# Kernel optimization log

Measured on AMD Instinct MI355X. Metric: run time of the kernel, lower is better.

The kernel has to match this reference:

```python
import jax, jax.numpy as jnp
import numpy as np

B, SX, SC, D, H = 4, 2048, 2048, 512, 8
DK = D // H


def setup_inputs() -> dict:
    key = jax.random.key(0)
    ks = jax.random.split(key, 12)
    s = 0.02
    return {
        "x": jax.random.normal(ks[0], (B, SX, D), jnp.float32),
        "c": jax.random.normal(ks[1], (B, SC, D), jnp.float32),
        "Wq": jax.random.normal(ks[2], (D, D), jnp.float32) * s,
        "bq": jnp.zeros((D,), jnp.float32),
        "Wk": jax.random.normal(ks[3], (D, D), jnp.float32) * s,
        "bk": jnp.zeros((D,), jnp.float32),
        "Wv": jax.random.normal(ks[4], (D, D), jnp.float32) * s,
        "bv": jnp.zeros((D,), jnp.float32),
        "Wo": jax.random.normal(ks[5], (D, D), jnp.float32) * s,
        "bo": jnp.zeros((D,), jnp.float32),
        "rel_table": jax.random.normal(ks[6], (SX + SC - 1, H), jnp.float32) * s,
    }


def reference(x, c, Wq, bq, Wk, bk, Wv, bv, Wo, bo, rel_table):
    b = x.shape[0]
    # projections (torch Linear: y = x @ W.T + b)
    q = (x @ Wq.T + bq).reshape(b, SX, H, DK).transpose(0, 2, 1, 3)  # (B,H,Sx,dk)
    k = (c @ Wk.T + bk).reshape(b, SC, H, DK).transpose(0, 2, 1, 3)  # (B,H,Sc,dk)
    v = (c @ Wv.T + bv).reshape(b, SC, H, DK).transpose(0, 2, 1, 3)
    scale = 1.0 / jnp.sqrt(jnp.float32(DK))
    scores = jnp.einsum('bhqd,bhkd->bhqk', q, k) * scale  # (B,H,Sx,Sc)
    # relative position bias: index (Sx,Sc) into table (Sx+Sc-1, H)
    rel_idx = jnp.arange(SX)[:, None] - jnp.arange(SC)[None, :] + (SC - 1)
    bias = rel_table[rel_idx].transpose(2, 0, 1)  # (H,Sx,Sc)
    scores = scores + bias[None]
    # causal_mask=False -> False * -1e9 adds 0 (no-op); omitted
    weights = jax.nn.softmax(scores, axis=-1)
    out = jnp.einsum('bhqk,bhkd->bhqd', weights, v)  # (B,H,Sx,dk)
    out = out.transpose(0, 2, 1, 3).reshape(b, SX, D)
    return out @ Wo.T + bo
```

## Files before the change

### kernel.cpp

```cpp
#include <hip/hip_runtime.h>
#include <hip/hip_bf16.h>
#include <cstdint>
#include <cstddef>

typedef __bf16 bf16;
typedef __bf16 bf16x4 __attribute__((ext_vector_type(4)));
typedef __bf16 bf16x8 __attribute__((ext_vector_type(8)));
typedef float f32x4 __attribute__((ext_vector_type(4)));
typedef float f32x16 __attribute__((ext_vector_type(16)));

#define MFMA16(a, b, c) __builtin_amdgcn_mfma_f32_16x16x32_bf16((a), (b), (c), 0, 0, 0)
#define MFMA32(a, b, c) __builtin_amdgcn_mfma_f32_32x32x16_bf16((a), (b), (c), 0, 0, 0)
#define GLD16(g, l) __builtin_amdgcn_global_load_lds( \
    (const __attribute__((address_space(1))) void*)(g), \
    (__attribute__((address_space(3))) void*)(l), 16, 0, 0)

constexpr int Bsz = 4, SX = 2048, SC = 2048, Dm = 512, H = 8, DK = 64;
constexpr float L2E = 1.4426950408889634f;

__global__ __launch_bounds__(256) void cvt_weights(
    const float* __restrict__ Wq, const float* __restrict__ Wk,
    const float* __restrict__ Wv, const float* __restrict__ Wo,
    bf16* __restrict__ out)
{
    int i = (blockIdx.x * 256 + threadIdx.x) * 8;
    int w = i >> 18;
    int off = i & 262143;
    const float* src = (w == 0) ? Wq : (w == 1) ? Wk : (w == 2) ? Wv : Wo;
    float4 v0 = *(const float4*)(src + off);
    float4 v1 = *(const float4*)(src + off + 4);
    bf16x8 o = { (bf16)v0.x, (bf16)v0.y, (bf16)v0.z, (bf16)v0.w,
                 (bf16)v1.x, (bf16)v1.y, (bf16)v1.z, (bf16)v1.w };
    *(bf16x8*)(out + i) = o;
}

__global__ __launch_bounds__(256) void cvt_xc(
    const float* __restrict__ x, const float* __restrict__ c,
    bf16* __restrict__ out)
{
    int i = (blockIdx.x * 256 + threadIdx.x) * 8;
    const float* src = (i < 4194304) ? x : c;
    int off = i & 4194303;
    float4 v0 = *(const float4*)(src + off);
    float4 v1 = *(const float4*)(src + off + 4);
    bf16x8 o = { (bf16)v0.x, (bf16)v0.y, (bf16)v0.z, (bf16)v0.w,
                 (bf16)v1.x, (bf16)v1.y, (bf16)v1.z, (bf16)v1.w };
    *(bf16x8*)(out + i) = o;
}

__global__ __launch_bounds__(256) void cvt_rel(
    const float* __restrict__ rel, float* __restrict__ relT)
{
    int h = blockIdx.y;
    int i = blockIdx.x * 256 + threadIdx.x;
    if (i < SX + SC - 1) relT[h * (SX + SC - 1) + i] = rel[i * H + h] * L2E;
}

template <int MODE>
__global__ __launch_bounds__(256, 2) void proj_gemm(
    const bf16* __restrict__ A, const bf16* __restrict__ W,
    const float* __restrict__ bias, void* __restrict__ Yv)
{
    __shared__ alignas(16) bf16 As[128 * 64];
    __shared__ alignas(16) bf16 Bs[128 * 64];

    const int t = threadIdx.x;
    const int n0 = blockIdx.x * 128;
    const int m0 = blockIdx.y * 128;
    const int wid = t >> 6, lane = t & 63, lr = lane & 15, lq = lane >> 4;
    const int wm = (wid & 1) * 64, wn = (wid >> 1) * 64;

    const int rl = lane >> 3;
    const int ch = (lane & 7) ^ rl;

    f32x4 acc[4][4];
#pragma unroll
    for (int i = 0; i < 4; i++)
#pragma unroll
        for (int j = 0; j < 4; j++) acc[i][j] = f32x4{0.f, 0.f, 0.f, 0.f};

    for (int k0 = 0; k0 < Dm; k0 += 64) {
        const bf16* ga = A + (size_t)(m0 + wid * 32 + rl) * Dm + k0 + ch * 8;
        const bf16* gb = W + (size_t)(n0 + wid * 32 + rl) * Dm + k0 + ch * 8;
#pragma unroll
        for (int g = 0; g < 4; g++)
            GLD16(ga + (size_t)g * 8 * Dm, &As[(wid * 32 + g * 8) * 64]);
#pragma unroll
        for (int g = 0; g < 4; g++)
            GLD16(gb + (size_t)g * 8 * Dm, &Bs[(wid * 32 + g * 8) * 64]);
        __syncthreads();
#pragma unroll
        for (int ks = 0; ks < 2; ks++) {
            bf16x8 af[4], bfr[4];
#pragma unroll
            for (int mt = 0; mt < 4; mt++)
                af[mt] = *(const bf16x8*)&As[(wm + mt * 16 + lr) * 64 + (((ks * 4 + lq) ^ (lr & 7)) * 8)];
#pragma unroll
            for (int nt = 0; nt < 4; nt++)
                bfr[nt] = *(const bf16x8*)&Bs[(wn + nt * 16 + lr) * 64 + (((ks * 4 + lq) ^ (lr & 7)) * 8)];
#pragma unroll
            for (int mt = 0; mt < 4; mt++)
#pragma unroll
                for (int nt = 0; nt < 4; nt++)
                    acc[mt][nt] = MFMA16(af[mt], bfr[nt], acc[mt][nt]);
        }
        __syncthreads();
    }

#pragma unroll
    for (int mt = 0; mt < 4; mt++) {
#pragma unroll
        for (int nt = 0; nt < 4; nt++) {
#pragma unroll
            for (int r = 0; r < 4; r++) {
                int m = m0 + wm + mt * 16 + lq * 4 + r;
                int n = n0 + wn + nt * 16 + lr;
                float v = acc[mt][nt][r] + bias[n];
                int bh = (m >> 11) * 8 + (n >> 6);
                int key = m & 2047, dk = n & 63;
                if constexpr (MODE == 0) {
                    ((bf16*)Yv)[(size_t)(bh * 2048 + key) * 64 + dk] = (bf16)v;
                } else if constexpr (MODE == 3) {
                    int idx = ((((bh * 64 + (key >> 5)) * 4 + (dk >> 4)) * 2 + ((dk >> 3) & 1)) * 32
                               + (key & 31)) * 8 + (dk & 7);
                    ((bf16*)Yv)[idx] = (bf16)v;
                } else if constexpr (MODE == 4) {
                    int idx = (((((bh * 32 + (key >> 6)) * 4 + ((key >> 4) & 3)) * 2 + (dk >> 5)) * 2
                                + ((key >> 3) & 1)) * 32 + (dk & 31)) * 8 + (key & 7);
                    ((bf16*)Yv)[idx] = (bf16)v;
                } else {
                    ((float*)Yv)[(size_t)m * Dm + n] = v;
                }
            }
        }
    }
}

constexpr int PST = 72;

__global__ __launch_bounds__(128, 4) void attn_kernel(
    const bf16* __restrict__ Qm, const bf16* __restrict__ Kf,
    const bf16* __restrict__ Vf, const float* __restrict__ relT,
    bf16* __restrict__ Oa)
{
    const int id = blockIdx.x;
    const int xcd = id & 7, j = id >> 3;
    const int bh = xcd + 8 * (j & 3);
    const int q0 = (j >> 2) * 32;
    const int h = bh & 7, b = bh >> 3;
    const int t = threadIdx.x;
    const int wid = t >> 6, lane = t & 63;
    const int l31 = lane & 31, l5 = lane >> 5;

    __shared__ alignas(16) char sm[19456];
    bf16*  Ps   = (bf16*)(sm + wid * 4608);
    float* Osum = (float*)(sm + 9216);
    float* Bsl  = (float*)(sm + 18432) + wid * 96;
    float* Ls1  = (float*)(sm + 19200);
    float* Lfin = (float*)(sm + 19328);

    const bf16* Qb = Qm + (size_t)bh * SC * DK;
    const bf16* Kb = Kf + (size_t)bh * 64 * 2048;
    const bf16* Vb = Vf + (size_t)bh * 32 * 4096;
    const float* rT = relT + h * (SX + SC - 1);

    bf16x8 qf[4];
#pragma unroll
    for (int ks = 0; ks < 4; ks++)
        qf[ks] = *(const bf16x8*)&Qb[(size_t)(q0 + l31) * DK + ks * 16 + l5 * 8];

    f32x16 oacc[2];
#pragma unroll
    for (int ng = 0; ng < 2; ng++)
#pragma unroll
        for (int r = 0; r < 16; r++) oacc[ng][r] = 0.f;
    float lsum = 0.f;

    const float sc = 0.125f * L2E;
    const int kw0 = wid << 10;

#pragma unroll 1
    for (int tt = 0; tt < 16; ++tt) {
        const int k0 = kw0 + tt * 64;
        int i0 = q0 - k0 + 1984;
        Bsl[lane] = rT[i0 + lane];
        if (lane < 31) Bsl[64 + lane] = rT[i0 + 64 + lane];

#pragma unroll
        for (int kg = 0; kg < 2; kg++) {
            const bf16* kb = Kb + (size_t)((k0 >> 5) + kg) * 2048 + lane * 8;
            f32x16 s;
#pragma unroll
            for (int r = 0; r < 16; r++) s[r] = 0.f;
#pragma unroll
            for (int ks = 0; ks < 4; ks++) {
                bf16x8 kf = *(const bf16x8*)(kb + ks * 512);
                s = MFMA32(kf, qf[ks], s);
            }
#pragma unroll
            for (int r4 = 0; r4 < 4; r4++) {
                float p[4];
#pragma unroll
                for (int r0 = 0; r0 < 4; r0++) {
                    int n = r0 + 8 * r4 + 4 * l5;
                    int ib = 63 + l31 - (kg * 32 + n);
                    p[r0] = __builtin_amdgcn_exp2f(s[r4 * 4 + r0] * sc + Bsl[ib]);
                    lsum += p[r0];
                }
                bf16x4 pk = { (bf16)p[0], (bf16)p[1], (bf16)p[2], (bf16)p[3] };
                *(bf16x4*)&Ps[l31 * PST + kg * 32 + 8 * r4 + 4 * l5] = pk;
            }
        }
        bf16x8 pf[4];
#pragma unroll
        for (int ks = 0; ks < 4; ks++)
            pf[ks] = *(const bf16x8*)&Ps[l31 * PST + ks * 16 + l5 * 8];
        const bf16* vb = Vb + (size_t)(k0 >> 6) * 4096 + lane * 8;
#pragma unroll
        for (int ng = 0; ng < 2; ng++) {
#pragma unroll
            for (int ks = 0; ks < 4; ks++) {
                bf16x8 vf = *(const bf16x8*)(vb + ng * 512 + ks * 1024);
                oacc[ng] = MFMA32(pf[ks], vf, oacc[ng]);
            }
        }
    }

    lsum += __shfl_xor(lsum, 32, 64);
    if (wid == 1) {
        if (lane < 32) Ls1[l31] = lsum;
        float* Op = Osum + lane * 36;
#pragma unroll
        for (int ng = 0; ng < 2; ng++)
#pragma unroll
            for (int q = 0; q < 4; q++) {
                f32x4 v = { oacc[ng][q * 4 + 0], oacc[ng][q * 4 + 1],
                            oacc[ng][q * 4 + 2], oacc[ng][q * 4 + 3] };
                *(f32x4*)(Op + ng * 16 + q * 4) = v;
            }
    }
    __syncthreads();
    if (wid == 0) {
        lsum += Ls1[l31];
        const float* Op = Osum + lane * 36;
#pragma unroll
        for (int ng = 0; ng < 2; ng++)
#pragma unroll
            for (int q = 0; q < 4; q++) {
                f32x4 v = *(const f32x4*)(Op + ng * 16 + q * 4);
#pragma unroll
                for (int r0 = 0; r0 < 4; r0++) oacc[ng][q * 4 + r0] += v[r0];
            }
        if (lane < 32) Lfin[l31] = lsum;
#pragma unroll
        for (int r4 = 0; r4 < 4; r4++) {
            float4 lv = *(const float4*)&Lfin[8 * r4 + 4 * l5];
            float rv[4] = { 1.f / lv.x, 1.f / lv.y, 1.f / lv.z, 1.f / lv.w };
#pragma unroll
            for (int ng = 0; ng < 2; ng++) {
#pragma unroll
                for (int r0 = 0; r0 < 4; r0++) {
                    int row = r0 + 8 * r4 + 4 * l5;
                    Oa[((size_t)(b * SX + q0 + row)) * Dm + h * 64 + ng * 32 + l31] =
                        (bf16)(oacc[ng][r4 * 4 + r0] * rv[r0]);
                }
            }
        }
    }
}

extern "C" void kernel_launch(void* const* d_in, const int* in_sizes, int n_in,
                              void* d_out, int out_size, void* d_ws, size_t ws_size,
                              hipStream_t stream)
{
    (void)in_sizes; (void)n_in; (void)out_size; (void)ws_size;

    const float* x   = (const float*)d_in[0];
    const float* c   = (const float*)d_in[1];
    const float* Wq  = (const float*)d_in[2];
    const float* bq  = (const float*)d_in[3];
    const float* Wk  = (const float*)d_in[4];
    const float* bk  = (const float*)d_in[5];
    const float* Wv  = (const float*)d_in[6];
    const float* bv  = (const float*)d_in[7];
    const float* Wo  = (const float*)d_in[8];
    const float* bo  = (const float*)d_in[9];
    const float* rel = (const float*)d_in[10];

    char* ws = (char*)d_ws;
    bf16*  Wbf  = (bf16*)ws;
    bf16*  Xbf  = (bf16*)(ws + (2u << 20));
    bf16*  Cbf  = Xbf + 4194304;
    bf16*  Aw   = (bf16*)(ws + (2u << 20));
    bf16*  Qw   = (bf16*)(ws + (18u << 20));
    bf16*  Kw   = (bf16*)(ws + (26u << 20));
    bf16*  Vw   = (bf16*)(ws + (34u << 20));
    float* relT = (float*)(ws + (42u << 20));

    cvt_weights<<<512, 256, 0, stream>>>(Wq, Wk, Wv, Wo, Wbf);
    cvt_xc<<<4096, 256, 0, stream>>>(x, c, Xbf);
    cvt_rel<<<dim3(16, 8), 256, 0, stream>>>(rel, relT);

    dim3 pg(4, 64);
    proj_gemm<0><<<pg, 256, 0, stream>>>(Xbf, Wbf + 0 * 262144, bq, Qw);
    proj_gemm<3><<<pg, 256, 0, stream>>>(Cbf, Wbf + 1 * 262144, bk, Kw);
    proj_gemm<4><<<pg, 256, 0, stream>>>(Cbf, Wbf + 2 * 262144, bv, Vw);

    attn_kernel<<<2048, 128, 0, stream>>>(Qw, Kw, Vw, relT, Aw);

    proj_gemm<2><<<pg, 256, 0, stream>>>(Aw, Wbf + 3 * 262144, bo, d_out);
}
```

Baseline: 219.0 us.

## Merge conversion and QKV projection launches, retile output GEMM, unroll attention loop

Folds the three conversion kernels into one launch and the three Q/K/V projection GEMMs into one grid of 768 blocks, with the projection chosen from blockIdx. The output projection becomes its own kernel with 64-row tiles, doubling the block count to fill more CUs. The attention tile loop is unrolled by 2. This cuts launch count and tail idle time at the cost of runtime branching in the fused GEMM epilogue and higher register pressure in attention.

New measurement: 205.2 us. 6.3% less time.

```diff
diff --git a/kernel.cpp b/kernel.cpp
--- a/kernel.cpp
+++ b/kernel.cpp
@@ -18,55 +18,59 @@
 constexpr int Bsz = 4, SX = 2048, SC = 2048, Dm = 512, H = 8, DK = 64;
 constexpr float L2E = 1.4426950408889634f;
 
-__global__ __launch_bounds__(256) void cvt_weights(
+__global__ __launch_bounds__(256) void cvt_all(
+    const float* __restrict__ x, const float* __restrict__ c,
     const float* __restrict__ Wq, const float* __restrict__ Wk,
     const float* __restrict__ Wv, const float* __restrict__ Wo,
-    bf16* __restrict__ out)
-{
-    int i = (blockIdx.x * 256 + threadIdx.x) * 8;
-    int w = i >> 18;
-    int off = i & 262143;
-    const float* src = (w == 0) ? Wq : (w == 1) ? Wk : (w == 2) ? Wv : Wo;
-    float4 v0 = *(const float4*)(src + off);
-    float4 v1 = *(const float4*)(src + off + 4);
-    bf16x8 o = { (bf16)v0.x, (bf16)v0.y, (bf16)v0.z, (bf16)v0.w,
-                 (bf16)v1.x, (bf16)v1.y, (bf16)v1.z, (bf16)v1.w };
-    *(bf16x8*)(out + i) = o;
-}
-
-__global__ __launch_bounds__(256) void cvt_xc(
-    const float* __restrict__ x, const float* __restrict__ c,
-    bf16* __restrict__ out)
-{
-    int i = (blockIdx.x * 256 + threadIdx.x) * 8;
-    const float* src = (i < 4194304) ? x : c;
-    int off = i & 4194303;
-    float4 v0 = *(const float4*)(src + off);
-    float4 v1 = *(const float4*)(src + off + 4);
-    bf16x8 o = { (bf16)v0.x, (bf16)v0.y, (bf16)v0.z, (bf16)v0.w,
-                 (bf16)v1.x, (bf16)v1.y, (bf16)v1.z, (bf16)v1.w };
-    *(bf16x8*)(out + i) = o;
-}
-
-__global__ __launch_bounds__(256) void cvt_rel(
-    const float* __restrict__ rel, float* __restrict__ relT)
-{
-    int h = blockIdx.y;
-    int i = blockIdx.x * 256 + threadIdx.x;
-    if (i < SX + SC - 1) relT[h * (SX + SC - 1) + i] = rel[i * H + h] * L2E;
-}
-
-template <int MODE>
-__global__ __launch_bounds__(256, 2) void proj_gemm(
-    const bf16* __restrict__ A, const bf16* __restrict__ W,
-    const float* __restrict__ bias, void* __restrict__ Yv)
+    const float* __restrict__ rel,
+    bf16* __restrict__ xcOut, bf16* __restrict__ wOut, float* __restrict__ relT)
+{
+    int blk = blockIdx.x;
+    if (blk < 4096) {
+        int i = (blk * 256 + threadIdx.x) * 8;
+        const float* src = (i < 4194304) ? x : c;
+        int off = i & 4194303;
+        float4 v0 = *(const float4*)(src + off);
+        float4 v1 = *(const float4*)(src + off + 4);
+        bf16x8 o = { (bf16)v0.x, (bf16)v0.y, (bf16)v0.z, (bf16)v0.w,
+                     (bf16)v1.x, (bf16)v1.y, (bf16)v1.z, (bf16)v1.w };
+        *(bf16x8*)(xcOut + i) = o;
+    } else if (blk < 4608) {
+        int i = ((blk - 4096) * 256 + threadIdx.x) * 8;
+        int w = i >> 18;
+        int off = i & 262143;
+        const float* src = (w == 0) ? Wq : (w == 1) ? Wk : (w == 2) ? Wv : Wo;
+        float4 v0 = *(const float4*)(src + off);
+        float4 v1 = *(const float4*)(src + off + 4);
+        bf16x8 o = { (bf16)v0.x, (bf16)v0.y, (bf16)v0.z, (bf16)v0.w,
+                     (bf16)v1.x, (bf16)v1.y, (bf16)v1.z, (bf16)v1.w };
+        *(bf16x8*)(wOut + i) = o;
+    } else {
+        int q = blk - 4608;
+        int h = q >> 4;
+        int i = (q & 15) * 256 + threadIdx.x;
+        if (i < SX + SC - 1) relT[h * (SX + SC - 1) + i] = rel[i * H + h] * L2E;
+    }
+}
+
+__global__ __launch_bounds__(256, 3) void qkv_gemm(
+    const bf16* __restrict__ Xbf, const bf16* __restrict__ Cbf,
+    const bf16* __restrict__ Wbf,
+    const float* __restrict__ bq, const float* __restrict__ bk,
+    const float* __restrict__ bv,
+    bf16* __restrict__ Qw, bf16* __restrict__ Kw, bf16* __restrict__ Vw)
 {
     __shared__ alignas(16) bf16 As[128 * 64];
     __shared__ alignas(16) bf16 Bs[128 * 64];
 
+    const int proj = blockIdx.x >> 2;
+    const int n0 = (blockIdx.x & 3) * 128;
+    const int m0 = blockIdx.y * 128;
+    const bf16* A = (proj == 0) ? Xbf : Cbf;
+    const bf16* W = Wbf + proj * 262144;
+    const float* bias = (proj == 0) ? bq : (proj == 1) ? bk : bv;
+
     const int t = threadIdx.x;
-    const int n0 = blockIdx.x * 128;
-    const int m0 = blockIdx.y * 128;
     const int wid = t >> 6, lane = t & 63, lr = lane & 15, lq = lane >> 4;
     const int wm = (wid & 1) * 64, wn = (wid >> 1) * 64;
 
@@ -118,19 +122,81 @@
                 float v = acc[mt][nt][r] + bias[n];
                 int bh = (m >> 11) * 8 + (n >> 6);
                 int key = m & 2047, dk = n & 63;
-                if constexpr (MODE == 0) {
-                    ((bf16*)Yv)[(size_t)(bh * 2048 + key) * 64 + dk] = (bf16)v;
-                } else if constexpr (MODE == 3) {
+                if (proj == 0) {
+                    Qw[(size_t)(bh * 2048 + key) * 64 + dk] = (bf16)v;
+                } else if (proj == 1) {
                     int idx = ((((bh * 64 + (key >> 5)) * 4 + (dk >> 4)) * 2 + ((dk >> 3) & 1)) * 32
                                + (key & 31)) * 8 + (dk & 7);
-                    ((bf16*)Yv)[idx] = (bf16)v;
-                } else if constexpr (MODE == 4) {
+                    Kw[idx] = (bf16)v;
+                } else {
                     int idx = (((((bh * 32 + (key >> 6)) * 4 + ((key >> 4) & 3)) * 2 + (dk >> 5)) * 2
                                 + ((key >> 3) & 1)) * 32 + (dk & 31)) * 8 + (key & 7);
-                    ((bf16*)Yv)[idx] = (bf16)v;
-                } else {
-                    ((float*)Yv)[(size_t)m * Dm + n] = v;
+                    Vw[idx] = (bf16)v;
                 }
+            }
+        }
+    }
+}
+
+__global__ __launch_bounds__(256, 2) void out_gemm(
+    const bf16* __restrict__ A, const bf16* __restrict__ W,
+    const float* __restrict__ bias, float* __restrict__ Y)
+{
+    __shared__ alignas(16) bf16 As[64 * 64];
+    __shared__ alignas(16) bf16 Bs[128 * 64];
+
+    const int t = threadIdx.x;
+    const int n0 = blockIdx.x * 128;
+    const int m0 = blockIdx.y * 64;
+    const int wid = t >> 6, lane = t & 63, lr = lane & 15, lq = lane >> 4;
+    const int wn = wid * 32;
+
+    const int rl = lane >> 3;
+    const int ch = (lane & 7) ^ rl;
+
+    f32x4 acc[4][2];
+#pragma unroll
+    for (int i = 0; i < 4; i++)
+#pragma unroll
+        for (int j = 0; j < 2; j++) acc[i][j] = f32x4{0.f, 0.f, 0.f, 0.f};
+
+    for (int k0 = 0; k0 < Dm; k0 += 64) {
+        const bf16* ga = A + (size_t)(m0 + wid * 16 + rl) * Dm + k0 + ch * 8;
+        const bf16* gb = W + (size_t)(n0 + wid * 32 + rl) * Dm + k0 + ch * 8;
+#pragma unroll
+        for (int g = 0; g < 2; g++)
+            GLD16(ga + (size_t)g * 8 * Dm, &As[(wid * 16 + g * 8) * 64]);
+#pragma unroll
+        for (int g = 0; g < 4; g++)
+            GLD16(gb + (size_t)g * 8 * Dm, &Bs[(wid * 32 + g * 8) * 64]);
+        __syncthreads();
+#pragma unroll
+        for (int ks = 0; ks < 2; ks++) {
+            bf16x8 af[4], bfr[2];
+#pragma unroll
+            for (int mt = 0; mt < 4; mt++)
+                af[mt] = *(const bf16x8*)&As[(mt * 16 + lr) * 64 + (((ks * 4 + lq) ^ (lr & 7)) * 8)];
+#pragma unroll
+            for (int nt = 0; nt < 2; nt++)
+                bfr[nt] = *(const bf16x8*)&Bs[(wn + nt * 16 + lr) * 64 + (((ks * 4 + lq) ^ (lr & 7)) * 8)];
+#pragma unroll
+            for (int mt = 0; mt < 4; mt++)
+#pragma unroll
+                for (int nt = 0; nt < 2; nt++)
+                    acc[mt][nt] = MFMA16(af[mt], bfr[nt], acc[mt][nt]);
+        }
+        __syncthreads();
+    }
+
+#pragma unroll
+    for (int mt = 0; mt < 4; mt++) {
+#pragma unroll
+        for (int nt = 0; nt < 2; nt++) {
+#pragma unroll
+            for (int r = 0; r < 4; r++) {
+                int m = m0 + mt * 16 + lq * 4 + r;
+                int n = n0 + wn + nt * 16 + lr;
+                Y[(size_t)m * Dm + n] = acc[mt][nt][r] + bias[n];
             }
         }
     }
@@ -179,7 +245,7 @@
     const float sc = 0.125f * L2E;
     const int kw0 = wid << 10;
 
-#pragma unroll 1
+#pragma unroll 2
     for (int tt = 0; tt < 16; ++tt) {
         const int k0 = kw0 + tt * 64;
         int i0 = q0 - k0 + 1984;
@@ -297,16 +363,11 @@
     bf16*  Vw   = (bf16*)(ws + (34u << 20));
     float* relT = (float*)(ws + (42u << 20));
 
-    cvt_weights<<<512, 256, 0, stream>>>(Wq, Wk, Wv, Wo, Wbf);
-    cvt_xc<<<4096, 256, 0, stream>>>(x, c, Xbf);
-    cvt_rel<<<dim3(16, 8), 256, 0, stream>>>(rel, relT);
-
-    dim3 pg(4, 64);
-    proj_gemm<0><<<pg, 256, 0, stream>>>(Xbf, Wbf + 0 * 262144, bq, Qw);
-    proj_gemm<3><<<pg, 256, 0, stream>>>(Cbf, Wbf + 1 * 262144, bk, Kw);
-    proj_gemm<4><<<pg, 256, 0, stream>>>(Cbf, Wbf + 2 * 262144, bv, Vw);
+    cvt_all<<<4736, 256, 0, stream>>>(x, c, Wq, Wk, Wv, Wo, rel, Xbf, Wbf, relT);
+
+    qkv_gemm<<<dim3(12, 64), 256, 0, stream>>>(Xbf, Cbf, Wbf, bq, bk, bv, Qw, Kw, Vw);
 
     attn_kernel<<<2048, 128, 0, stream>>>(Qw, Kw, Vw, relT, Aw);
 
-    proj_gemm<2><<<pg, 256, 0, stream>>>(Aw, Wbf + 3 * 262144, bo, d_out);
-}
+    out_gemm<<<dim3(4, 128), 256, 0, stream>>>(Aw, Wbf + 3 * 262144, bo, (float*)d_out);
+}
```
